# Performance work log

Measured on AMD Instinct MI355X. Metric: run time of the kernel, lower is better.

Reference implementation:

```python
import jax, jax.numpy as jnp
import numpy as np

B, D, E = 128, 1024, 1024   # batch, word_rnn_size, word_encoding_size
NV, NL = 36, 20             # visual regions, language memory slots
T = 4                       # max_att_step
EPS = 0.01                  # opt.epsilon
SCALE = 0.02


def _lstm_cell(x, h, c, Wih, Whh, bih, bhh):
    # torch.nn.LSTMCell gate order: i, f, g, o
    g = x @ Wih.T + bih + h @ Whh.T + bhh
    i, f, gg, o = jnp.split(g, 4, axis=-1)
    c2 = jax.nn.sigmoid(f) * c + jax.nn.sigmoid(i) * jnp.tanh(gg)
    h2 = jax.nn.sigmoid(o) * jnp.tanh(c2)
    return h2, c2


def _kv_attention(h_att, vkey, vval, lkey, lval, kvs):
    # stand-in for the externally-passed kv_attention module:
    # scaled dot-product attention over visual and language memories
    q = h_att + kvs                                   # [B,D]
    inv = 1.0 / np.sqrt(D)
    va = jax.nn.softmax(jnp.einsum('bnd,bd->bn', vkey, q) * inv, axis=-1)
    vctx = jnp.einsum('bn,bnd->bd', va, vval)
    la = jax.nn.softmax(jnp.einsum('bmd,bd->bm', lkey, q) * inv, axis=-1)
    lctx = jnp.einsum('bm,bmd->bd', la, lval)
    return vctx, lctx, jnp.tanh(kvs + vctx + lctx)


def _update_kv(out, vkey, lkey):
    # stand-in for the externally-passed update_kv module
    return vkey + 0.01 * out[:, None, :], lkey + 0.01 * out[:, None, :]


def _forward(xt, fc_feats, visual_value, visual_key, lang_value, lang_key,
             kv_state, state_h, state_c,
             att_Wih, att_Whh, att_bih, att_bhh,
             lang_Wih, lang_Whh, lang_bih, lang_bhh,
             conf_W1, conf_b1, conf_W2, conf_b2,
             it, max_att_step):
    word_exist = (it > 0).astype(jnp.float32)         # [B]
    prev_h = state_h[-1]
    # att_lstm input is constant across halting steps (state is not updated in the loop)
    att_in = jnp.concatenate([prev_h, fc_feats, xt], axis=1)  # [B, E+2D]
    z1 = jnp.zeros((B, 1), jnp.float32)
    zD = jnp.zeros((B, D), jnp.float32)
    zB = jnp.zeros((B,), jnp.float32)
    carry0 = (z1, jnp.ones((B, 1), jnp.float32), zD, zD, zD, zD, zD, zB,
              visual_key, lang_key, kv_state)

    def body(carry, i):
        accum, sel, hA, cA, hL, cL, outA, cost, vkey, lkey, kvs = carry
        h_att, c_att = _lstm_cell(att_in, state_h[0], state_c[0],
                                  att_Wih, att_Whh, att_bih, att_bhh)
        vctx, lctx, kvs = _kv_attention(h_att, vkey, visual_value, lkey, lang_value, kvs)
        lang_in = jnp.concatenate([vctx, lctx, h_att], axis=1)  # [B,3D]
        h_lang, c_lang = _lstm_cell(lang_in, state_h[1], state_c[1],
                                    lang_Wih, lang_Whh, lang_bih, lang_bhh)
        out = h_lang  # F.dropout in eval mode is identity
        vkey, lkey = _update_kv(out, vkey, lkey)
        # confidence MLP: Linear -> ReLU -> Linear -> Sigmoid
        p = jax.nn.sigmoid(jax.nn.relu(h_lang @ conf_W1.T + conf_b1) @ conf_W2.T + conf_b2)  # [B,1]
        beta = p * (1.0 - accum)
        accum = accum + beta * sel
        hA = hA + beta * h_att * sel
        cA = cA + beta * c_att * sel
        hL = hL + beta * h_lang * sel
        cL = cL + beta * c_lang * sel
        outA = outA + beta * out * sel
        cost = cost + (i + 1.0) * (1.0 - p[:, 0]) * sel[:, 0]
        sel = jax.lax.stop_gradient((accum < 1.0 - EPS).astype(jnp.float32)) * sel
        return (accum, sel, hA, cA, hL, cL, outA, cost, vkey, lkey, kvs), None

    carry, _ = jax.lax.scan(body, carry0, jnp.arange(max_att_step, dtype=jnp.float32))
    accum, sel, hA, cA, hL, cL, outA, cost, vkey, lkey, kvs = carry
    hA = hA / accum
    cA = cA / accum
    hL = hL / accum
    cL = cL / accum
    outA = outA / accum
    new_h = jnp.stack([hA, hL])
    new_c = jnp.stack([cA, cL])
    return outA, vkey, lkey, cost * word_exist, new_h, new_c, kvs


def setup_inputs() -> dict:
    ks = jax.random.split(jax.random.key(0), 20)
    n = lambda k, s, sc=1.0: jax.random.normal(k, s, dtype=jnp.float32) * sc
    return {
        'xt': n(ks[0], (B, E)),
        'it': jax.random.randint(ks[1], (B,), 0, 9487, dtype=jnp.int32),
        'fc_feats': n(ks[2], (B, D)),
        'visual_value': n(ks[3], (B, NV, D)),
        'visual_key': n(ks[4], (B, NV, D)),
        'lang_value': n(ks[5], (B, NL, D)),
        'lang_key': n(ks[6], (B, NL, D)),
        'kv_state': n(ks[7], (B, D)),
        'state_h': n(ks[8], (2, B, D)),
        'state_c': n(ks[9], (2, B, D)),
        'max_att_step': T,
        'att_Wih': n(ks[10], (4 * D, E + 2 * D), SCALE),
        'att_Whh': n(ks[11], (4 * D, D), SCALE),
        'att_bih': jnp.zeros((4 * D,), jnp.float32),
        'att_bhh': jnp.zeros((4 * D,), jnp.float32),
        'lang_Wih': n(ks[12], (4 * D, 3 * D), SCALE),
        'lang_Whh': n(ks[13], (4 * D, D), SCALE),
        'lang_bih': jnp.zeros((4 * D,), jnp.float32),
        'lang_bhh': jnp.zeros((4 * D,), jnp.float32),
        'conf_W1': n(ks[14], (D, D), SCALE),
        'conf_b1': jnp.zeros((D,), jnp.float32),
        'conf_W2': n(ks[15], (1, D), SCALE),
        'conf_b2': jnp.zeros((1,), jnp.float32),
    }


def reference(xt, it, fc_feats, visual_value, visual_key, lang_value, lang_key,
              kv_state, state_h, state_c, max_att_step,
              att_Wih, att_Whh, att_bih, att_bhh,
              lang_Wih, lang_Whh, lang_bih, lang_bhh,
              conf_W1, conf_b1, conf_W2, conf_b2):
    return _forward(xt, fc_feats, visual_value, visual_key, lang_value, lang_key,
                    kv_state, state_h, state_c,
                    att_Wih, att_Whh, att_bih, att_bhh,
                    lang_Wih, lang_Whh, lang_bih, lang_bhh,
                    conf_W1, conf_b1, conf_W2, conf_b2,
                    it, max_att_step)
```

## Files before the change

kernel.cpp:

```cpp
#include <hip/hip_runtime.h>
#include <hip/hip_bf16.h>

constexpr int B  = 128;
constexpr int D  = 1024;
constexpr int NV = 36;
constexpr int NL = 20;
constexpr int BD = B * D;
constexpr float EPS = 0.01f;
constexpr int NSLOT = 8;

constexpr long SL  = 524288;
constexpr long SLB = 2097152;
constexpr long OFF_GPA   = 0;
constexpr long OFF_GPLB  = OFF_GPA + 8 * SL;
constexpr long OFF_LBASE = OFF_GPLB + 8 * SL;
constexpr long OFF_GPB   = OFF_LBASE + SL;
constexpr long OFF_GPC0  = OFF_GPB + 2 * SLB;
constexpr long OFF_GPC1  = OFF_GPC0 + 524288;
constexpr long OFF_HATT2 = OFF_GPC1 + 524288;
constexpr long OFF_HLB   = OFF_HATT2 + BD;
constexpr long OFF_CLB   = OFF_HLB + 524288;
constexpr long OFF_S2    = OFF_CLB + 524288;
constexpr long OFF_VVB   = OFF_S2 + BD;
constexpr long OFF_LVB   = OFF_VVB + 2359296;
constexpr long OFF_VKB   = OFF_LVB + 1310720;
constexpr long OFF_LKB   = OFF_VKB + 2359296;
constexpr long OFF_HATB  = OFF_LKB + 1310720;
constexpr long OFF_SH1B  = OFF_HATB + 65536;
constexpr long OFF_VCXB  = OFF_SH1B + 65536;
constexpr long OFF_LCXB  = OFF_VCXB + 262144;

typedef float f32x4 __attribute__((ext_vector_type(4)));
typedef short s16x8 __attribute__((ext_vector_type(8)));

__device__ __forceinline__ float sigf(float x) { return 1.f / (1.f + expf(-x)); }

__device__ __forceinline__ short f2bf(float f) {
  __hip_bfloat16 h = __float2bfloat16(f);
  return *reinterpret_cast<short*>(&h);
}
__device__ __forceinline__ float bf2f(short s) {
  unsigned u = ((unsigned)(unsigned short)s) << 16;
  return __uint_as_float(u);
}

__device__ __forceinline__ f32x4 LD4(const float* p) { return *(const f32x4*)p; }
__device__ __forceinline__ void ST4(float* p, f32x4 v) { *(f32x4*)p = v; }

__device__ __forceinline__ void conv_bf16(const float* __restrict__ src,
                                          __hip_bfloat16* __restrict__ dst,
                                          long nelem) {
  const long total = nelem >> 2;
  for (long i = (long)blockIdx.x * 256 + threadIdx.x; i < total;
       i += (long)gridDim.x * 256) {
    f32x4 v = LD4(src + i * 4);
    *(short4*)((short*)dst + i * 4) =
        short4{f2bf(v[0]), f2bf(v[1]), f2bf(v[2]), f2bf(v[3])};
  }
}

__global__ __launch_bounds__(256) void conv_kv(
    const float* __restrict__ vkey, const float* __restrict__ lkey,
    const float* __restrict__ vval, const float* __restrict__ lval,
    const float* __restrict__ sh1,
    __hip_bfloat16* __restrict__ vkb, __hip_bfloat16* __restrict__ lkb,
    __hip_bfloat16* __restrict__ vvb, __hip_bfloat16* __restrict__ lvb,
    __hip_bfloat16* __restrict__ sh1b) {
  conv_bf16(vkey, vkb, (long)B * NV * 1024);
  conv_bf16(lkey, lkb, (long)B * NL * 1024);
  conv_bf16(vval, vvb, (long)B * NV * 1024);
  conv_bf16(lval, lvb, (long)B * NL * 1024);
  conv_bf16(sh1, sh1b, (long)BD);
}

struct GemmArgs {
  const void* A[NSLOT];
  const float* W[NSLOT];
  long wstride[NSLOT];
  int abf16[NSLOT];
  int klen;
};

__global__ __launch_bounds__(256, 2) void gemm_mfma(GemmArgs ga, int N,
                                                    long pstride,
                                                    float* __restrict__ gpart) {
  __shared__ __align__(16) short As[2][128][72];
  __shared__ __align__(16) short Bs[2][128][72];
  const int z = blockIdx.z;
  const int ab = ga.abf16[z];
  const float* __restrict__ Af = (const float*)ga.A[z];
  const short* __restrict__ Ah = (const short*)ga.A[z];
  const float* __restrict__ W = ga.W[z];
  const long wstr = ga.wstride[z];
  const int brow = blockIdx.y * 128;
  const int bcol = blockIdx.x * 128;
  float* __restrict__ out = gpart + (long)z * pstride;

  const int tid = threadIdx.x;
  const int wave = tid >> 6, lane = tid & 63;
  const int wr = wave >> 1, wc = wave & 1;
  const int lrow = lane & 15;
  const int lk8  = (lane >> 4) * 8;
  const int sr = tid >> 4;
  const int sc4 = (tid & 15) * 4;
  const int br8 = tid >> 3;
  (void)br8;

  f32x4 acc[4][4];
#pragma unroll
  for (int m = 0; m < 4; ++m)
#pragma unroll
    for (int n = 0; n < 4; ++n) acc[m][n] = (f32x4){0.f, 0.f, 0.f, 0.f};

  float4 ra[8], rw[8];
  s16x8 rab[4];
#define LOAD_TILE(KT)                                                          \
  {                                                                            \
    const int kb = (KT) * 64;                                                  \
    if (ab) {                                                                  \
      _Pragma("unroll") for (int i = 0; i < 4; ++i) {                          \
        const int idx = tid + i * 256;                                         \
        const int r = idx >> 3, c8 = (idx & 7) * 8;                            \
        rab[i] = *(const s16x8*)(Ah + (long)(brow + r) * 1024 + kb + c8);      \
      }                                                                        \
    } else {                                                                   \
      _Pragma("unroll") for (int i = 0; i < 8; ++i) {                          \
        const int r = sr + i * 16;                                             \
        ra[i] = *(const float4*)(Af + (long)(brow + r) * 1024 + kb + sc4);     \
      }                                                                        \
    }                                                                          \
    _Pragma("unroll") for (int i = 0; i < 8; ++i) {                            \
      const int r = sr + i * 16;                                               \
      rw[i] = *(const float4*)(W + (long)(bcol + r) * wstr + kb + sc4);        \
    }                                                                          \
  }
#define WRITE_TILE(BUF)                                                        \
  {                                                                            \
    if (ab) {                                                                  \
      _Pragma("unroll") for (int i = 0; i < 4; ++i) {                          \
        const int idx = tid + i * 256;                                         \
        const int r = idx >> 3, c8 = (idx & 7) * 8;                            \
        *(s16x8*)(&As[BUF][r][c8]) = rab[i];                                   \
      }                                                                        \
    } else {                                                                   \
      _Pragma("unroll") for (int i = 0; i < 8; ++i) {                          \
        const int r = sr + i * 16;                                             \
        *(short4*)(&As[BUF][r][sc4]) =                                         \
            short4{f2bf(ra[i].x), f2bf(ra[i].y), f2bf(ra[i].z), f2bf(ra[i].w)};\
      }                                                                        \
    }                                                                          \
    _Pragma("unroll") for (int i = 0; i < 8; ++i) {                            \
      const int r = sr + i * 16;                                               \
      *(short4*)(&Bs[BUF][r][sc4]) =                                           \
          short4{f2bf(rw[i].x), f2bf(rw[i].y), f2bf(rw[i].z), f2bf(rw[i].w)};  \
    }                                                                          \
  }

  const int ntiles = ga.klen / 64;
  LOAD_TILE(0);
  WRITE_TILE(0);
  __syncthreads();
  for (int kt = 0; kt < ntiles; ++kt) {
    const int cur = kt & 1;
    const bool more = (kt + 1 < ntiles);
    if (more) LOAD_TILE(kt + 1);
#pragma unroll
    for (int kk = 0; kk < 64; kk += 32) {
      s16x8 af[4], bf[4];
#pragma unroll
      for (int m = 0; m < 4; ++m)
        af[m] = *(const s16x8*)(&As[cur][wr * 64 + m * 16 + lrow][kk + lk8]);
#pragma unroll
      for (int n = 0; n < 4; ++n)
        bf[n] = *(const s16x8*)(&Bs[cur][wc * 64 + n * 16 + lrow][kk + lk8]);
#pragma unroll
      for (int m = 0; m < 4; ++m)
#pragma unroll
        for (int n = 0; n < 4; ++n)
          acc[m][n] = __builtin_amdgcn_mfma_f32_16x16x32_bf16(
              af[m], bf[n], acc[m][n], 0, 0, 0);
    }
    if (more) WRITE_TILE(1 - cur);
    __syncthreads();
  }
#undef LOAD_TILE
#undef WRITE_TILE

#pragma unroll
  for (int m = 0; m < 4; ++m) {
#pragma unroll
    for (int n = 0; n < 4; ++n) {
      const int col = bcol + wc * 64 + n * 16 + lrow;
#pragma unroll
      for (int r = 0; r < 4; ++r) {
        const int row = brow + wr * 64 + m * 16 + (lane >> 4) * 4 + r;
        out[(long)row * N + col] = acc[m][n][r];
      }
    }
  }
}

constexpr long O1 = BD;
constexpr long O2 = O1 + (long)B * NV * D;
constexpr long O3 = O2 + (long)B * NL * D;
constexpr long O4 = O3 + B;
constexpr long O5 = O4 + 2L * BD;
constexpr long O6 = O5 + 2L * BD;
constexpr long O7 = O6 + BD;

__global__ __launch_bounds__(256) void lstm_att(
    const float* __restrict__ gp, const float* __restrict__ bih,
    const float* __restrict__ bhh, const float* __restrict__ c_prev,
    float* __restrict__ h, __hip_bfloat16* __restrict__ hb,
    float* __restrict__ out) {
  long idx = ((long)blockIdx.x * 256 + threadIdx.x) * 4;
  if (idx >= BD) return;
  int b = (int)(idx >> 10), d = (int)(idx & 1023);
  const long base = (long)b * 4096 + d;
  f32x4 g[4];
#pragma unroll
  for (int gi = 0; gi < 4; ++gi) {
    const long o = base + gi * 1024;
    f32x4 v = LD4(bih + gi * 1024 + d) + LD4(bhh + gi * 1024 + d);
#pragma unroll
    for (int s = 0; s < NSLOT; ++s) v += LD4(gp + s * SL + o);
    g[gi] = v;
  }
  f32x4 cp = LD4(c_prev + idx), cc, hh;
#pragma unroll
  for (int j = 0; j < 4; ++j) {
    float ccj = sigf(g[1][j]) * cp[j] + sigf(g[0][j]) * tanhf(g[2][j]);
    cc[j] = ccj;
    hh[j] = sigf(g[3][j]) * tanhf(ccj);
  }
  ST4(h + idx, hh);
  *(short4*)((short*)hb + idx) =
      short4{f2bf(hh[0]), f2bf(hh[1]), f2bf(hh[2]), f2bf(hh[3])};
  ST4(out + O4 + idx, hh);
  ST4(out + O5 + idx, cc);
}

__global__ __launch_bounds__(256) void reduce8(
    const float* __restrict__ gp, const float* __restrict__ bih,
    const float* __restrict__ bhh, float* __restrict__ out) {
  long idx = ((long)blockIdx.x * 256 + threadIdx.x) * 4;
  if (idx >= (long)B * 4096) return;
  int col = (int)(idx & 4095);
  f32x4 v = LD4(bih + col) + LD4(bhh + col);
#pragma unroll
  for (int s = 0; s < NSLOT; ++s) v += LD4(gp + s * SL + idx);
  ST4(out + idx, v);
}

__global__ __launch_bounds__(1024) void attn_mega(
    const float* __restrict__ h_att, const float* __restrict__ kv0,
    const __hip_bfloat16* __restrict__ vkb, const __hip_bfloat16* __restrict__ lkb,
    const __hip_bfloat16* __restrict__ vvb, const __hip_bfloat16* __restrict__ lvb,
    __hip_bfloat16* __restrict__ vctxB, __hip_bfloat16* __restrict__ lctxB,
    float* __restrict__ out_kvs) {
  const int b = blockIdx.x, tid = threadIdx.x;
  __shared__ short K[56][1024];
  __shared__ float q[1024];
  __shared__ float wgt[64];
  const int wave = tid >> 6, lane = tid & 63;

  for (int i = tid; i < 56 * 128; i += 1024) {
    const int r = i >> 7, c8 = (i & 127) * 8;
    const __hip_bfloat16* kp = (r < NV)
        ? vkb + ((long)b * NV + r) * 1024
        : lkb + ((long)b * NL + (r - NV)) * 1024;
    *(s16x8*)(&K[r][c8]) = *(const s16x8*)(kp + c8);
  }

  const float ha = h_att[(long)b * 1024 + tid];
  float kv = kv0[(long)b * 1024 + tid];

  for (int step = 0; step < 4; ++step) {
    q[tid] = ha + kv;
    __syncthreads();
    for (int n = wave; n < NV + NL; n += 16) {
      float s = 0.f;
#pragma unroll
      for (int j = 0; j < 2; ++j) {
        const int base = lane * 8 + j * 512;
        s16x8 k8 = *(const s16x8*)(&K[n][base]);
        f32x4 q0 = *(const f32x4*)(&q[base]);
        f32x4 q1 = *(const f32x4*)(&q[base + 4]);
#pragma unroll
        for (int e = 0; e < 4; ++e) {
          s += bf2f(k8[e]) * q0[e];
          s += bf2f(k8[e + 4]) * q1[e];
        }
      }
      for (int m = 32; m >= 1; m >>= 1) s += __shfl_xor(s, m);
      if (lane == 0) wgt[n] = s * (1.0f / 32.0f);
    }
    __syncthreads();
    if (wave == 0) {
      float x = (lane < NV) ? wgt[lane] : -1e30f;
      float m = x;
      for (int k = 32; k >= 1; k >>= 1) m = fmaxf(m, __shfl_xor(m, k));
      float e = (lane < NV) ? expf(x - m) : 0.f;
      float ssum = e;
      for (int k = 32; k >= 1; k >>= 1) ssum += __shfl_xor(ssum, k);
      if (lane < NV) wgt[lane] = e / ssum;
    } else if (wave == 1) {
      float x = (lane < NL) ? wgt[NV + lane] : -1e30f;
      float m = x;
      for (int k = 32; k >= 1; k >>= 1) m = fmaxf(m, __shfl_xor(m, k));
      float e = (lane < NL) ? expf(x - m) : 0.f;
      float ssum = e;
      for (int k = 32; k >= 1; k >>= 1) ssum += __shfl_xor(ssum, k);
      if (lane < NL) wgt[NV + lane] = e / ssum;
    }
    __syncthreads();
    const __hip_bfloat16* vb = vvb + (long)b * NV * 1024 + tid;
    float a0 = 0.f, a1 = 0.f, a2 = 0.f, a3 = 0.f;
#pragma unroll
    for (int n = 0; n < NV; n += 4) {
      a0 += __bfloat162float(vb[(long)(n + 0) * 1024]) * wgt[n + 0];
      a1 += __bfloat162float(vb[(long)(n + 1) * 1024]) * wgt[n + 1];
      a2 += __bfloat162float(vb[(long)(n + 2) * 1024]) * wgt[n + 2];
      a3 += __bfloat162float(vb[(long)(n + 3) * 1024]) * wgt[n + 3];
    }
    const float vc = (a0 + a1) + (a2 + a3);
    const __hip_bfloat16* lb = lvb + (long)b * NL * 1024 + tid;
    float c0 = 0.f, c1 = 0.f, c2 = 0.f, c3 = 0.f;
#pragma unroll
    for (int n = 0; n < NL; n += 4) {
      c0 += __bfloat162float(lb[(long)(n + 0) * 1024]) * wgt[NV + n + 0];
      c1 += __bfloat162float(lb[(long)(n + 1) * 1024]) * wgt[NV + n + 1];
      c2 += __bfloat162float(lb[(long)(n + 2) * 1024]) * wgt[NV + n + 2];
      c3 += __bfloat162float(lb[(long)(n + 3) * 1024]) * wgt[NV + n + 3];
    }
    const float lc = (c0 + c1) + (c2 + c3);
    const long orow = ((long)step * 128 + b) * 1024 + tid;
    vctxB[orow] = __float2bfloat16(vc);
    lctxB[orow] = __float2bfloat16(lc);
    kv = tanhf(kv + vc + lc);
    __syncthreads();
  }
  out_kvs[(long)b * 1024 + tid] = kv;
}

__global__ __launch_bounds__(256) void lstm_batch(
    const float* __restrict__ gpB, const float* __restrict__ lbase,
    const float* __restrict__ sc1, float* __restrict__ hB,
    float* __restrict__ cB) {
  long idx = ((long)blockIdx.x * 256 + threadIdx.x) * 4;
  if (idx >= 512L * 1024) return;
  const int row = (int)(idx >> 10);
  const int b = row & 127;
  const int d = (int)(idx & 1023);
  const long base = (long)row * 4096 + d;
  const long lbbase = (long)b * 4096 + d;
  f32x4 g[4];
#pragma unroll
  for (int gi = 0; gi < 4; ++gi) {
    const long o = gi * 1024;
    g[gi] = LD4(gpB + base + o) + LD4(gpB + SLB + base + o) +
            LD4(lbase + lbbase + o);
  }
  f32x4 cp = LD4(sc1 + (long)b * 1024 + d), cc, hh;
#pragma unroll
  for (int j = 0; j < 4; ++j) {
    float ccj = sigf(g[1][j]) * cp[j] + sigf(g[0][j]) * tanhf(g[2][j]);
    cc[j] = ccj;
    hh[j] = sigf(g[3][j]) * tanhf(ccj);
  }
  ST4(cB + idx, cc);
  ST4(hB + idx, hh);
}

__global__ __launch_bounds__(256) void halt_scan(
    const float* __restrict__ gpc0, const float* __restrict__ gpc1,
    const float* __restrict__ cb1, const float* __restrict__ W2,
    const float* __restrict__ b2, const float* __restrict__ hB,
    const float* __restrict__ cB, const int* __restrict__ it,
    float* __restrict__ Sout, float* __restrict__ out) {
  const int b = blockIdx.x, tid = threadIdx.x;
  const int d0 = tid * 4;
  __shared__ float red[256];
  __shared__ float p_sh;
  const f32x4 w4 = LD4(W2 + d0);
  const f32x4 cb = LD4(cb1 + d0);
  f32x4 hl_acc = (f32x4){0.f, 0.f, 0.f, 0.f}, cl_acc = hl_acc, s_acc = hl_acc;
  float a = 0.f, sel = 1.f, cost = 0.f;

  for (int i = 0; i < 4; ++i) {
    const long o = ((long)i * 128 + b) * 1024 + d0;
    f32x4 rv = LD4(gpc0 + o) + LD4(gpc1 + o) + cb;
    float part = 0.f;
#pragma unroll
    for (int j = 0; j < 4; ++j) part += fmaxf(rv[j], 0.f) * w4[j];
    red[tid] = part;
    __syncthreads();
    for (int s = 128; s > 0; s >>= 1) {
      if (tid < s) red[tid] += red[tid + s];
      __syncthreads();
    }
    if (tid == 0) p_sh = sigf(red[0] + b2[0]);
    __syncthreads();
    const float p = p_sh;
    const float bs = p * (1.f - a) * sel;
    f32x4 hl = LD4(hB + o), cl = LD4(cB + o);
    hl_acc += hl * bs;
    cl_acc += cl * bs;
    s_acc += hl;
    cost += (float)(i + 1) * (1.f - p) * sel;
    a += bs;
    sel = (a < 1.f - EPS) ? sel : 0.f;
    __syncthreads();
  }
  const float inv_a = 1.f / a;
  const long ob = (long)b * 1024 + d0;
  ST4(out + ob, hl_acc * inv_a);
  ST4(out + O4 + BD + ob, hl_acc * inv_a);
  ST4(out + O5 + BD + ob, cl_acc * inv_a);
  ST4(Sout + ob, s_acc);
  if (tid == 0) out[O3 + b] = cost * ((it[b] > 0) ? 1.f : 0.f);
}

constexpr long VK = (long)B * NV * D;
constexpr long LK = (long)B * NL * D;

__global__ __launch_bounds__(256) void finalize2(
    const __hip_bfloat16* __restrict__ vkb, const __hip_bfloat16* __restrict__ lkb,
    const float* __restrict__ S, float* __restrict__ out) {
  long idx = ((long)blockIdx.x * 256 + threadIdx.x) * 8;
  if (idx < VK) {
    int b = (int)(idx / (NV * 1024));
    int d = (int)(idx & 1023);
    s16x8 k8 = *(const s16x8*)((const short*)vkb + idx);
    f32x4 s0 = LD4(S + (long)b * 1024 + d), s1 = LD4(S + (long)b * 1024 + d + 4);
    f32x4 o0, o1;
#pragma unroll
    for (int j = 0; j < 4; ++j) {
      o0[j] = bf2f(k8[j]) + 0.01f * s0[j];
      o1[j] = bf2f(k8[j + 4]) + 0.01f * s1[j];
    }
    ST4(out + O1 + idx, o0);
    ST4(out + O1 + idx + 4, o1);
  } else if (idx < VK + LK) {
    long r = idx - VK;
    int b = (int)(r / (NL * 1024));
    int d = (int)(r & 1023);
    s16x8 k8 = *(const s16x8*)((const short*)lkb + r);
    f32x4 s0 = LD4(S + (long)b * 1024 + d), s1 = LD4(S + (long)b * 1024 + d + 4);
    f32x4 o0, o1;
#pragma unroll
    for (int j = 0; j < 4; ++j) {
      o0[j] = bf2f(k8[j]) + 0.01f * s0[j];
      o1[j] = bf2f(k8[j + 4]) + 0.01f * s1[j];
    }
    ST4(out + O2 + r, o0);
    ST4(out + O2 + r + 4, o1);
  }
}

extern "C" void kernel_launch(void* const* d_in, const int* in_sizes, int n_in,
                              void* d_out, int out_size, void* d_ws, size_t ws_size,
                              hipStream_t stream) {
  const float* xt   = (const float*)d_in[0];
  const int*   it   = (const int*)d_in[1];
  const float* fc   = (const float*)d_in[2];
  const float* vval = (const float*)d_in[3];
  const float* vkey = (const float*)d_in[4];
  const float* lval = (const float*)d_in[5];
  const float* lkey = (const float*)d_in[6];
  const float* kv0  = (const float*)d_in[7];
  const float* sh   = (const float*)d_in[8];
  const float* sc   = (const float*)d_in[9];
  const float* aWih = (const float*)d_in[11];
  const float* aWhh = (const float*)d_in[12];
  const float* abih = (const float*)d_in[13];
  const float* abhh = (const float*)d_in[14];
  const float* lWih = (const float*)d_in[15];
  const float* lWhh = (const float*)d_in[16];
  const float* lbih = (const float*)d_in[17];
  const float* lbhh = (const float*)d_in[18];
  const float* cW1  = (const float*)d_in[19];
  const float* cb1  = (const float*)d_in[20];
  const float* cW2  = (const float*)d_in[21];
  const float* cb2  = (const float*)d_in[22];

  float* ws = (float*)d_ws;
  float* gpA   = ws + OFF_GPA;
  float* gpLB  = ws + OFF_GPLB;
  float* lbase = ws + OFF_LBASE;
  float* gpB   = ws + OFF_GPB;
  float* gpC0  = ws + OFF_GPC0;
  float* gpC1  = ws + OFF_GPC1;
  float* h_att = ws + OFF_HATT2;
  float* hB    = ws + OFF_HLB;
  float* cB    = ws + OFF_CLB;
  float* Sbuf  = ws + OFF_S2;
  __hip_bfloat16* vvb  = (__hip_bfloat16*)(ws + OFF_VVB);
  __hip_bfloat16* lvb  = (__hip_bfloat16*)(ws + OFF_LVB);
  __hip_bfloat16* vkb  = (__hip_bfloat16*)(ws + OFF_VKB);
  __hip_bfloat16* lkb  = (__hip_bfloat16*)(ws + OFF_LKB);
  __hip_bfloat16* hatb = (__hip_bfloat16*)(ws + OFF_HATB);
  __hip_bfloat16* sh1b = (__hip_bfloat16*)(ws + OFF_SH1B);
  __hip_bfloat16* vcxb = (__hip_bfloat16*)(ws + OFF_VCXB);
  __hip_bfloat16* lcxb = (__hip_bfloat16*)(ws + OFF_LCXB);

  const float* sh1 = sh + BD;
  const float* sc0 = sc;
  const float* sc1 = sc + BD;
  float* out = (float*)d_out;

  conv_kv<<<2048, 256, 0, stream>>>(vkey, lkey, vval, lval, sh1,
                                    vkb, lkb, vvb, lvb, sh1b);

  {
    GemmArgs ga = {};
    ga.A[0] = sh1;       ga.W[0] = aWih;        ga.wstride[0] = 3072;
    ga.A[1] = sh1 + 512; ga.W[1] = aWih + 512;  ga.wstride[1] = 3072;
    ga.A[2] = fc;        ga.W[2] = aWih + 1024; ga.wstride[2] = 3072;
    ga.A[3] = fc + 512;  ga.W[3] = aWih + 1536; ga.wstride[3] = 3072;
    ga.A[4] = xt;        ga.W[4] = aWih + 2048; ga.wstride[4] = 3072;
    ga.A[5] = xt + 512;  ga.W[5] = aWih + 2560; ga.wstride[5] = 3072;
    ga.A[6] = sh;        ga.W[6] = aWhh;        ga.wstride[6] = 1024;
    ga.A[7] = sh + 512;  ga.W[7] = aWhh + 512;  ga.wstride[7] = 1024;
    ga.klen = 512;
    gemm_mfma<<<dim3(32, 1, 8), 256, 0, stream>>>(ga, 4096, SL, gpA);
  }
  lstm_att<<<128, 256, 0, stream>>>(gpA, abih, abhh, sc0, h_att, hatb, out);

  attn_mega<<<128, 1024, 0, stream>>>(h_att, kv0, vkb, lkb, vvb, lvb,
                                      vcxb, lcxb, out + O6);

  {
    GemmArgs ga = {};
#pragma unroll
    for (int q = 0; q < 4; ++q) {
      ga.A[q] = (const void*)((const short*)sh1b + q * 256);
      ga.W[q] = lWhh + q * 256;
      ga.wstride[q] = 1024;
      ga.abf16[q] = 1;
      ga.A[4 + q] = (const void*)((const short*)hatb + q * 256);
      ga.W[4 + q] = lWih + 2048 + q * 256;
      ga.wstride[4 + q] = 3072;
      ga.abf16[4 + q] = 1;
    }
    ga.klen = 256;
    gemm_mfma<<<dim3(32, 1, 8), 256, 0, stream>>>(ga, 4096, SL, gpLB);
  }
  reduce8<<<512, 256, 0, stream>>>(gpLB, lbih, lbhh, lbase);

  {
    GemmArgs ga = {};
    ga.A[0] = vcxb; ga.W[0] = lWih;        ga.wstride[0] = 3072; ga.abf16[0] = 1;
    ga.A[1] = lcxb; ga.W[1] = lWih + 1024; ga.wstride[1] = 3072; ga.abf16[1] = 1;
    ga.klen = 1024;
    gemm_mfma<<<dim3(32, 4, 2), 256, 0, stream>>>(ga, 4096, SLB, gpB);
  }
  lstm_batch<<<512, 256, 0, stream>>>(gpB, lbase, sc1, hB, cB);

  {
    GemmArgs ga = {};
    ga.A[0] = hB;       ga.W[0] = cW1;       ga.wstride[0] = 1024;
    ga.A[1] = hB + 512; ga.W[1] = cW1 + 512; ga.wstride[1] = 1024;
    ga.klen = 512;
    gemm_mfma<<<dim3(8, 4, 2), 256, 0, stream>>>(ga, 1024, 524288, gpC0);
  }
  halt_scan<<<128, 256, 0, stream>>>(gpC0, gpC1, cb1, cW2, cb2, hB, cB, it,
                                     Sbuf, out);
  finalize2<<<3584, 256, 0, stream>>>(vkb, lkb, Sbuf, out);
}
```

Measured before the change: 155.4 us.

## Use 512-thread GEMM blocks and deeper split-K across all GEMM stages

The MFMA GEMM kernel moves from 4 waves to 8 waves per 128x128 tile, with each wave now covering a 64x32 sub-tile and the tile loads spread over 512 threads. Split-K is also doubled for the att-LSTM, lang-batch and confidence GEMMs (16, 4 and 4 partial slots), and the reduction kernels now sum more partials. The aim is more waves and blocks in flight on a GPU that is underfilled at batch 128, at the cost of more partial-sum traffic and extra reduction work.

```diff
diff --git a/kernel.cpp b/kernel.cpp
--- a/kernel.cpp
+++ b/kernel.cpp
@@ -7,17 +7,17 @@
 constexpr int NL = 20;
 constexpr int BD = B * D;
 constexpr float EPS = 0.01f;
-constexpr int NSLOT = 8;
+constexpr int NSLOT = 16;
 
 constexpr long SL  = 524288;
 constexpr long SLB = 2097152;
+constexpr long SLC = 524288;
 constexpr long OFF_GPA   = 0;
-constexpr long OFF_GPLB  = OFF_GPA + 8 * SL;
+constexpr long OFF_GPLB  = OFF_GPA + 16 * SL;
 constexpr long OFF_LBASE = OFF_GPLB + 8 * SL;
 constexpr long OFF_GPB   = OFF_LBASE + SL;
-constexpr long OFF_GPC0  = OFF_GPB + 2 * SLB;
-constexpr long OFF_GPC1  = OFF_GPC0 + 524288;
-constexpr long OFF_HATT2 = OFF_GPC1 + 524288;
+constexpr long OFF_GPC   = OFF_GPB + 4 * SLB;
+constexpr long OFF_HATT2 = OFF_GPC + 4 * SLC;
 constexpr long OFF_HLB   = OFF_HATT2 + BD;
 constexpr long OFF_CLB   = OFF_HLB + 524288;
 constexpr long OFF_S2    = OFF_CLB + 524288;
@@ -81,7 +81,7 @@
   int klen;
 };
 
-__global__ __launch_bounds__(256, 2) void gemm_mfma(GemmArgs ga, int N,
+__global__ __launch_bounds__(512, 4) void gemm_mfma(GemmArgs ga, int N,
                                                     long pstride,
                                                     float* __restrict__ gpart) {
   __shared__ __align__(16) short As[2][128][72];
@@ -98,60 +98,60 @@
 
   const int tid = threadIdx.x;
   const int wave = tid >> 6, lane = tid & 63;
-  const int wr = wave >> 1, wc = wave & 1;
+  const int wr = wave >> 2, wc = wave & 3;
   const int lrow = lane & 15;
   const int lk8  = (lane >> 4) * 8;
-  const int sr = tid >> 4;
-  const int sc4 = (tid & 15) * 4;
-  const int br8 = tid >> 3;
-  (void)br8;
-
-  f32x4 acc[4][4];
+
+  f32x4 acc[4][2];
 #pragma unroll
   for (int m = 0; m < 4; ++m)
 #pragma unroll
-    for (int n = 0; n < 4; ++n) acc[m][n] = (f32x4){0.f, 0.f, 0.f, 0.f};
-
-  float4 ra[8], rw[8];
-  s16x8 rab[4];
+    for (int n = 0; n < 2; ++n) acc[m][n] = (f32x4){0.f, 0.f, 0.f, 0.f};
+
+  float4 ra[4], rw[4];
+  s16x8 rab[2];
 #define LOAD_TILE(KT)                                                          \
   {                                                                            \
     const int kb = (KT) * 64;                                                  \
     if (ab) {                                                                  \
-      _Pragma("unroll") for (int i = 0; i < 4; ++i) {                          \
-        const int idx = tid + i * 256;                                         \
+      _Pragma("unroll") for (int i = 0; i < 2; ++i) {                          \
+        const int idx = tid + i * 512;                                         \
         const int r = idx >> 3, c8 = (idx & 7) * 8;                            \
         rab[i] = *(const s16x8*)(Ah + (long)(brow + r) * 1024 + kb + c8);      \
       }                                                                        \
     } else {                                                                   \
-      _Pragma("unroll") for (int i = 0; i < 8; ++i) {                          \
-        const int r = sr + i * 16;                                             \
-        ra[i] = *(const float4*)(Af + (long)(brow + r) * 1024 + kb + sc4);     \
+      _Pragma("unroll") for (int i = 0; i < 4; ++i) {                          \
+        const int idx = tid + i * 512;                                         \
+        const int r = idx >> 4, c4 = (idx & 15) * 4;                           \
+        ra[i] = *(const float4*)(Af + (long)(brow + r) * 1024 + kb + c4);      \
       }                                                                        \
     }                                                                          \
-    _Pragma("unroll") for (int i = 0; i < 8; ++i) {                            \
-      const int r = sr + i * 16;                                               \
-      rw[i] = *(const float4*)(W + (long)(bcol + r) * wstr + kb + sc4);        \
+    _Pragma("unroll") for (int i = 0; i < 4; ++i) {                            \
+      const int idx = tid + i * 512;                                           \
+      const int r = idx >> 4, c4 = (idx & 15) * 4;                             \
+      rw[i] = *(const float4*)(W + (long)(bcol + r) * wstr + kb + c4);         \
     }                                                                          \
   }
 #define WRITE_TILE(BUF)                                                        \
   {                                                                            \
     if (ab) {                                                                  \
-      _Pragma("unroll") for (int i = 0; i < 4; ++i) {                          \
-        const int idx = tid + i * 256;                                         \
+      _Pragma("unroll") for (int i = 0; i < 2; ++i) {                          \
+        const int idx = tid + i * 512;                                         \
         const int r = idx >> 3, c8 = (idx & 7) * 8;                            \
         *(s16x8*)(&As[BUF][r][c8]) = rab[i];                                   \
       }                                                                        \
     } else {                                                                   \
-      _Pragma("unroll") for (int i = 0; i < 8; ++i) {                          \
-        const int r = sr + i * 16;                                             \
-        *(short4*)(&As[BUF][r][sc4]) =                                         \
+      _Pragma("unroll") for (int i = 0; i < 4; ++i) {                          \
+        const int idx = tid + i * 512;                                         \
+        const int r = idx >> 4, c4 = (idx & 15) * 4;                           \
+        *(short4*)(&As[BUF][r][c4]) =                                          \
             short4{f2bf(ra[i].x), f2bf(ra[i].y), f2bf(ra[i].z), f2bf(ra[i].w)};\
       }                                                                        \
     }                                                                          \
-    _Pragma("unroll") for (int i = 0; i < 8; ++i) {                            \
-      const int r = sr + i * 16;                                               \
-      *(short4*)(&Bs[BUF][r][sc4]) =                                           \
+    _Pragma("unroll") for (int i = 0; i < 4; ++i) {                            \
+      const int idx = tid + i * 512;                                           \
+      const int r = idx >> 4, c4 = (idx & 15) * 4;                             \
+      *(short4*)(&Bs[BUF][r][c4]) =                                            \
           short4{f2bf(rw[i].x), f2bf(rw[i].y), f2bf(rw[i].z), f2bf(rw[i].w)};  \
     }                                                                          \
   }
@@ -166,17 +166,17 @@
     if (more) LOAD_TILE(kt + 1);
 #pragma unroll
     for (int kk = 0; kk < 64; kk += 32) {
-      s16x8 af[4], bf[4];
+      s16x8 af[4], bf[2];
 #pragma unroll
       for (int m = 0; m < 4; ++m)
         af[m] = *(const s16x8*)(&As[cur][wr * 64 + m * 16 + lrow][kk + lk8]);
 #pragma unroll
-      for (int n = 0; n < 4; ++n)
-        bf[n] = *(const s16x8*)(&Bs[cur][wc * 64 + n * 16 + lrow][kk + lk8]);
+      for (int n = 0; n < 2; ++n)
+        bf[n] = *(const s16x8*)(&Bs[cur][wc * 32 + n * 16 + lrow][kk + lk8]);
 #pragma unroll
       for (int m = 0; m < 4; ++m)
 #pragma unroll
-        for (int n = 0; n < 4; ++n)
+        for (int n = 0; n < 2; ++n)
           acc[m][n] = __builtin_amdgcn_mfma_f32_16x16x32_bf16(
               af[m], bf[n], acc[m][n], 0, 0, 0);
     }
@@ -189,8 +189,8 @@
 #pragma unroll
   for (int m = 0; m < 4; ++m) {
 #pragma unroll
-    for (int n = 0; n < 4; ++n) {
-      const int col = bcol + wc * 64 + n * 16 + lrow;
+    for (int n = 0; n < 2; ++n) {
+      const int col = bcol + wc * 32 + n * 16 + lrow;
 #pragma unroll
       for (int r = 0; r < 4; ++r) {
         const int row = brow + wr * 64 + m * 16 + (lane >> 4) * 4 + r;
@@ -223,7 +223,7 @@
     const long o = base + gi * 1024;
     f32x4 v = LD4(bih + gi * 1024 + d) + LD4(bhh + gi * 1024 + d);
 #pragma unroll
-    for (int s = 0; s < NSLOT; ++s) v += LD4(gp + s * SL + o);
+    for (int s = 0; s < 16; ++s) v += LD4(gp + s * SL + o);
     g[gi] = v;
   }
   f32x4 cp = LD4(c_prev + idx), cc, hh;
@@ -248,7 +248,7 @@
   int col = (int)(idx & 4095);
   f32x4 v = LD4(bih + col) + LD4(bhh + col);
 #pragma unroll
-  for (int s = 0; s < NSLOT; ++s) v += LD4(gp + s * SL + idx);
+  for (int s = 0; s < 8; ++s) v += LD4(gp + s * SL + idx);
   ST4(out + idx, v);
 }
 
@@ -358,8 +358,10 @@
 #pragma unroll
   for (int gi = 0; gi < 4; ++gi) {
     const long o = gi * 1024;
-    g[gi] = LD4(gpB + base + o) + LD4(gpB + SLB + base + o) +
-            LD4(lbase + lbbase + o);
+    f32x4 v = LD4(lbase + lbbase + o);
+#pragma unroll
+    for (int s = 0; s < 4; ++s) v += LD4(gpB + s * SLB + base + o);
+    g[gi] = v;
   }
   f32x4 cp = LD4(sc1 + (long)b * 1024 + d), cc, hh;
 #pragma unroll
@@ -373,11 +375,11 @@
 }
 
 __global__ __launch_bounds__(256) void halt_scan(
-    const float* __restrict__ gpc0, const float* __restrict__ gpc1,
-    const float* __restrict__ cb1, const float* __restrict__ W2,
-    const float* __restrict__ b2, const float* __restrict__ hB,
-    const float* __restrict__ cB, const int* __restrict__ it,
-    float* __restrict__ Sout, float* __restrict__ out) {
+    const float* __restrict__ gpc, const float* __restrict__ cb1,
+    const float* __restrict__ W2, const float* __restrict__ b2,
+    const float* __restrict__ hB, const float* __restrict__ cB,
+    const int* __restrict__ it, float* __restrict__ Sout,
+    float* __restrict__ out) {
   const int b = blockIdx.x, tid = threadIdx.x;
   const int d0 = tid * 4;
   __shared__ float red[256];
@@ -389,7 +391,9 @@
 
   for (int i = 0; i < 4; ++i) {
     const long o = ((long)i * 128 + b) * 1024 + d0;
-    f32x4 rv = LD4(gpc0 + o) + LD4(gpc1 + o) + cb;
+    f32x4 rv = cb;
+#pragma unroll
+    for (int s = 0; s < 4; ++s) rv += LD4(gpc + s * SLC + o);
     float part = 0.f;
 #pragma unroll
     for (int j = 0; j < 4; ++j) part += fmaxf(rv[j], 0.f) * w4[j];
@@ -489,8 +493,7 @@
   float* gpLB  = ws + OFF_GPLB;
   float* lbase = ws + OFF_LBASE;
   float* gpB   = ws + OFF_GPB;
-  float* gpC0  = ws + OFF_GPC0;
-  float* gpC1  = ws + OFF_GPC1;
+  float* gpC   = ws + OFF_GPC;
   float* h_att = ws + OFF_HATT2;
   float* hB    = ws + OFF_HLB;
   float* cB    = ws + OFF_CLB;
@@ -514,16 +517,17 @@
 
   {
     GemmArgs ga = {};
-    ga.A[0] = sh1;       ga.W[0] = aWih;        ga.wstride[0] = 3072;
-    ga.A[1] = sh1 + 512; ga.W[1] = aWih + 512;  ga.wstride[1] = 3072;
-    ga.A[2] = fc;        ga.W[2] = aWih + 1024; ga.wstride[2] = 3072;
-    ga.A[3] = fc + 512;  ga.W[3] = aWih + 1536; ga.wstride[3] = 3072;
-    ga.A[4] = xt;        ga.W[4] = aWih + 2048; ga.wstride[4] = 3072;
-    ga.A[5] = xt + 512;  ga.W[5] = aWih + 2560; ga.wstride[5] = 3072;
-    ga.A[6] = sh;        ga.W[6] = aWhh;        ga.wstride[6] = 1024;
-    ga.A[7] = sh + 512;  ga.W[7] = aWhh + 512;  ga.wstride[7] = 1024;
-    ga.klen = 512;
-    gemm_mfma<<<dim3(32, 1, 8), 256, 0, stream>>>(ga, 4096, SL, gpA);
+    const float* Aops[4] = {sh1, fc, xt, sh};
+    const float* Wops[4] = {aWih, aWih + 1024, aWih + 2048, aWhh};
+    const long wstrs[4] = {3072, 3072, 3072, 1024};
+    for (int p = 0; p < 4; ++p)
+      for (int q = 0; q < 4; ++q) {
+        ga.A[p * 4 + q] = Aops[p] + q * 256;
+        ga.W[p * 4 + q] = Wops[p] + q * 256;
+        ga.wstride[p * 4 + q] = wstrs[p];
+      }
+    ga.klen = 256;
+    gemm_mfma<<<dim3(32, 1, 16), 512, 0, stream>>>(ga, 4096, SL, gpA);
   }
   lstm_att<<<128, 256, 0, stream>>>(gpA, abih, abhh, sc0, h_att, hatb, out);
 
@@ -532,7 +536,6 @@
 
   {
     GemmArgs ga = {};
-#pragma unroll
     for (int q = 0; q < 4; ++q) {
       ga.A[q] = (const void*)((const short*)sh1b + q * 256);
       ga.W[q] = lWhh + q * 256;
@@ -544,27 +547,36 @@
       ga.abf16[4 + q] = 1;
     }
     ga.klen = 256;
-    gemm_mfma<<<dim3(32, 1, 8), 256, 0, stream>>>(ga, 4096, SL, gpLB);
+    gemm_mfma<<<dim3(32, 1, 8), 512, 0, stream>>>(ga, 4096, SL, gpLB);
   }
   reduce8<<<512, 256, 0, stream>>>(gpLB, lbih, lbhh, lbase);
 
   {
     GemmArgs ga = {};
-    ga.A[0] = vcxb; ga.W[0] = lWih;        ga.wstride[0] = 3072; ga.abf16[0] = 1;
-    ga.A[1] = lcxb; ga.W[1] = lWih + 1024; ga.wstride[1] = 3072; ga.abf16[1] = 1;
-    ga.klen = 1024;
-    gemm_mfma<<<dim3(32, 4, 2), 256, 0, stream>>>(ga, 4096, SLB, gpB);
+    ga.A[0] = vcxb;                              ga.W[0] = lWih;
+    ga.wstride[0] = 3072; ga.abf16[0] = 1;
+    ga.A[1] = (const void*)((const short*)vcxb + 512); ga.W[1] = lWih + 512;
+    ga.wstride[1] = 3072; ga.abf16[1] = 1;
+    ga.A[2] = lcxb;                              ga.W[2] = lWih + 1024;
+    ga.wstride[2] = 3072; ga.abf16[2] = 1;
+    ga.A[3] = (const void*)((const short*)lcxb + 512); ga.W[3] = lWih + 1536;
+    ga.wstride[3] = 3072; ga.abf16[3] = 1;
+    ga.klen = 512;
+    gemm_mfma<<<dim3(32, 4, 4), 512, 0, stream>>>(ga, 4096, SLB, gpB);
   }
   lstm_batch<<<512, 256, 0, stream>>>(gpB, lbase, sc1, hB, cB);
 
   {
     GemmArgs ga = {};
-    ga.A[0] = hB;       ga.W[0] = cW1;       ga.wstride[0] = 1024;
-    ga.A[1] = hB + 512; ga.W[1] = cW1 + 512; ga.wstride[1] = 1024;
-    ga.klen = 512;
-    gemm_mfma<<<dim3(8, 4, 2), 256, 0, stream>>>(ga, 1024, 524288, gpC0);
-  }
-  halt_scan<<<128, 256, 0, stream>>>(gpC0, gpC1, cb1, cW2, cb2, hB, cB, it,
+    for (int q = 0; q < 4; ++q) {
+      ga.A[q] = hB + q * 256;
+      ga.W[q] = cW1 + q * 256;
+      ga.wstride[q] = 1024;
+    }
+    ga.klen = 256;
+    gemm_mfma<<<dim3(8, 4, 4), 512, 0, stream>>>(ga, 1024, SLC, gpC);
+  }
+  halt_scan<<<128, 256, 0, stream>>>(gpC, cb1, cW2, cb2, hB, cB, it,
                                      Sbuf, out);
   finalize2<<<3584, 256, 0, stream>>>(vkb, lkb, Sbuf, out);
 }
```

Result: no change. 156.3 us (+0.6%).
